# Kernel tuning notes

Measured on AMD Instinct MI355X. Metric: run time of the kernel, lower is better.

## Reference

```python
import jax, jax.numpy as jnp
import numpy as np

DN = ('NCHW', 'OIHW', 'NCHW')

def conv2d(x, w, b, stride, pad):
    y = jax.lax.conv_general_dilated(x, w, (stride, stride), [(pad, pad), (pad, pad)], dimension_numbers=DN)
    return y + b[None, :, None, None]

def convT2d(x, w, b, stride, pad):
    # w is torch ConvTranspose2d layout (in, out, kh, kw)
    k = w.shape[2]
    w2 = jnp.flip(w, (2, 3)).transpose(1, 0, 2, 3)  # -> (out, in, kh, kw)
    p = k - 1 - pad
    y = jax.lax.conv_general_dilated(x, w2, (1, 1), [(p, p), (p, p)], lhs_dilation=(stride, stride), dimension_numbers=DN)
    return y + b[None, :, None, None]

def setup_inputs() -> dict:
    key = jax.random.key(0)
    ks = jax.random.split(key, 24)
    s = 0.05
    inp = {
        'x': jax.random.uniform(ks[0], (16, 3, 256, 256), jnp.float32),
        'enc_w1': jax.random.normal(ks[1], (64, 3, 4, 4)) * s,   'enc_b1': jnp.zeros((64,)),
        'enc_w2': jax.random.normal(ks[2], (128, 64, 4, 4)) * s, 'enc_b2': jnp.zeros((128,)),
        'enc_w3': jax.random.normal(ks[3], (256, 128, 3, 3)) * s,'enc_b3': jnp.zeros((256,)),
        'enc_w4': jax.random.normal(ks[4], (256, 256, 3, 3)) * s,'enc_b4': jnp.zeros((256,)),
        'codebooks': jax.random.normal(ks[5], (4, 1024, 256)) * s,
        'dec_w1': jax.random.normal(ks[6], (128, 256, 3, 3)) * s,'dec_b1': jnp.zeros((128,)),
        'dec_w2': jax.random.normal(ks[7], (128, 64, 4, 4)) * s, 'dec_b2': jnp.zeros((64,)),
        'dec_w3': jax.random.normal(ks[8], (64, 64, 4, 4)) * s,  'dec_b3': jnp.zeros((64,)),
        'dec_w4': jax.random.normal(ks[9], (64, 3, 4, 4)) * s,   'dec_b4': jnp.zeros((3,)),
    }
    return inp

def residual_vq(zf, codebooks):
    # zf: (N, C) flattened tokens; codebooks: (Q, K, C)
    residual = zf
    q_out = jnp.zeros_like(zf)
    losses, inds = [], []
    for i in range(codebooks.shape[0]):
        cb = codebooks[i]  # (K, C)
        # squared distance up to a constant |r|^2 term (same argmin)
        d = jnp.sum(cb * cb, -1)[None, :] - 2.0 * (residual @ cb.T)  # (N, K)
        idx = jnp.argmin(d, axis=-1)  # (N,)
        q = cb[idx]  # (N, C)
        losses.append(jnp.mean((jax.lax.stop_gradient(q) - residual) ** 2))
        q_st = residual + jax.lax.stop_gradient(q - residual)  # straight-through
        q_out = q_out + q_st
        residual = residual - jax.lax.stop_gradient(q)
        inds.append(idx)
    return q_out, jnp.stack(inds, -1), jnp.stack(losses)

def reference(x, enc_w1, enc_b1, enc_w2, enc_b2, enc_w3, enc_b3, enc_w4, enc_b4,
              codebooks, dec_w1, dec_b1, dec_w2, dec_b2, dec_w3, dec_b3, dec_w4, dec_b4):
    h = jax.nn.relu(conv2d(x, enc_w1, enc_b1, 2, 1))
    h = jax.nn.relu(conv2d(h, enc_w2, enc_b2, 2, 1))
    h = jax.nn.relu(conv2d(h, enc_w3, enc_b3, 1, 1))
    z = conv2d(h, enc_w4, enc_b4, 1, 1)  # (B, C, H, W)
    B, C, H, W = z.shape
    zf = z.transpose(0, 2, 3, 1).reshape(B * H * W, C)
    qf, idx, commit_loss = residual_vq(zf, codebooks)
    quantized = qf.reshape(B, H, W, C).transpose(0, 3, 1, 2)
    # indices: (B, HW, Q) -> permute(0,2,1) -> view(B, Q, H, W)
    Q = codebooks.shape[0]
    indices = idx.reshape(B, H * W, Q).transpose(0, 2, 1).reshape(B, Q, H, W)
    d = jax.nn.relu(conv2d(quantized, dec_w1, dec_b1, 1, 1))
    d = jax.nn.relu(convT2d(d, dec_w2, dec_b2, 2, 1))
    d = jax.nn.relu(convT2d(d, dec_w3, dec_b3, 2, 1))
    recon = jnp.tanh(convT2d(d, dec_w4, dec_b4, 2, 1))
    return (recon, indices, commit_loss, quantized)
```

## Files before the change

### kernel.cpp

```cpp
#include <hip/hip_runtime.h>
#include <cmath>


typedef unsigned short u16;
typedef unsigned int   u32;
typedef __attribute__((ext_vector_type(8))) short s16x8;
typedef __attribute__((ext_vector_type(4))) short s16x4;
typedef __attribute__((ext_vector_type(4))) float f32x4;
typedef __attribute__((address_space(1))) const u32 gu32;
typedef __attribute__((address_space(3))) u32 lu32;

__device__ __forceinline__ u16 f2bf(float v) {
  u32 b = __builtin_bit_cast(u32, v);
  b += 0x7FFFu + ((b >> 16) & 1u);
  return (u16)(b >> 16);
}
__device__ __forceinline__ float bf2f(u16 h) {
  u32 b = ((u32)h) << 16;
  return __builtin_bit_cast(float, b);
}

template<int RW>
__device__ __forceinline__ void load_row(const float* __restrict__ p, float* r) {
  if constexpr (RW == 5) {
    float4 a = *(const float4*)p;
    r[0]=a.x; r[1]=a.y; r[2]=a.z; r[3]=a.w; r[4]=p[4];
  } else if constexpr (RW == 6) {
    float4 a = *(const float4*)p; float2 b = *(const float2*)(p+4);
    r[0]=a.x; r[1]=a.y; r[2]=a.z; r[3]=a.w; r[4]=b.x; r[5]=b.y;
  } else if constexpr (RW == 10) {
    float4 a = *(const float4*)p; float4 b = *(const float4*)(p+4);
    float2 c = *(const float2*)(p+8);
    r[0]=a.x; r[1]=a.y; r[2]=a.z; r[3]=a.w;
    r[4]=b.x; r[5]=b.y; r[6]=b.z; r[7]=b.w; r[8]=c.x; r[9]=c.y;
  }
}

template<int OCT, int SPTH, int SPTW, int KH, int KW, int S, int ACT>
__global__ __launch_bounds__(256) void conv_tiled(
    const float* __restrict__ in, const float* __restrict__ wgt,
    const float* __restrict__ bias, float* __restrict__ out,
    int N, int Cin, int Hin, int Win, int Cout, int WT,
    int padY, int padX,
    long outBase, long outNStride, long outCStride, long outYStride, long outXStride)
{
  constexpr int CK   = 8;
  constexpr int IH   = (SPTH-1)*S + KH;
  constexpr int IWr  = (SPTW-1)*S + KW;
  constexpr int IW   = (IWr + 3) & ~3;
  constexpr int TAPS = KH*KW;
  constexpr int WST  = (OCT==64) ? 68 : 5;
  constexpr int LOC  = (OCT==64) ? 16 : 4;
  constexpr int OPT  = OCT/LOC;
  constexpr int RW   = 3*S + KW;
  constexpr int EPW  = (OCT==64) ? 65 : 257;
  constexpr int SP   = SPTH*SPTW;
  constexpr int STG  = CK*IH*IW + CK*TAPS*WST;
  constexpr int SMEMN = (STG > OCT*EPW) ? STG : OCT*EPW;
  __shared__ float smem[SMEMN];
  float* s_in = smem;
  float* s_w  = smem + CK*IH*IW;

  const int tid  = threadIdx.x;
  const int tile = blockIdx.x, ocb = blockIdx.y, n = blockIdx.z;
  const int oy0 = (tile / WT) * SPTH, ox0 = (tile % WT) * SPTW;
  const int ol  = tid % LOC;
  const int g   = tid / LOC;
  const int s0  = g * 4;
  const int sy  = s0 / SPTW, sx0 = s0 % SPTW;
  const int iy0 = oy0*S - padY, ix0 = ox0*S - padX;

  float acc[OPT][4];
#pragma unroll
  for (int o = 0; o < OPT; ++o)
#pragma unroll
    for (int j = 0; j < 4; ++j) acc[o][j] = 0.f;

  for (int c0 = 0; c0 < Cin; c0 += CK) {
    __syncthreads();
    for (int i = tid; i < CK*IH*IW; i += 256) {
      int c = i / (IH*IW), r2 = i % (IH*IW);
      int iy = r2 / IW, ix = r2 % IW;
      int gy = iy0 + iy, gx = ix0 + ix;
      float v = 0.f;
      if (c0 + c < Cin && (unsigned)gy < (unsigned)Hin && (unsigned)gx < (unsigned)Win)
        v = in[(((long)n*Cin + c0 + c)*Hin + gy)*Win + gx];
      s_in[i] = v;
    }
    for (int i = tid; i < OCT*CK*TAPS; i += 256) {
      int o = i / (CK*TAPS), ct = i % (CK*TAPS);
      int oc = ocb*OCT + o, ci = c0 + ct / TAPS;
      float v = 0.f;
      if (oc < Cout && ci < Cin)
        v = wgt[((long)oc*Cin + ci)*TAPS + (ct % TAPS)];
      s_w[ct*WST + o] = v;
    }
    __syncthreads();

    for (int c = 0; c < CK; ++c) {
#pragma unroll
      for (int ky = 0; ky < KH; ++ky) {
        float r[RW];
        load_row<RW>(&s_in[c*(IH*IW) + (sy*S + ky)*IW + sx0*S], r);
#pragma unroll
        for (int kx = 0; kx < KW; ++kx) {
          if constexpr (OCT == 64) {
            float4 w4 = *(const float4*)&s_w[(c*TAPS + ky*KW + kx)*WST + ol*4];
            float wv[4] = {w4.x, w4.y, w4.z, w4.w};
#pragma unroll
            for (int o = 0; o < 4; ++o)
#pragma unroll
              for (int j = 0; j < 4; ++j)
                acc[o][j] = fmaf(wv[o], r[j*S + kx], acc[o][j]);
          } else {
            float w = s_w[(c*TAPS + ky*KW + kx)*WST + ol];
#pragma unroll
            for (int j = 0; j < 4; ++j)
              acc[0][j] = fmaf(w, r[j*S + kx], acc[0][j]);
          }
        }
      }
    }
  }

  __syncthreads();
#pragma unroll
  for (int o = 0; o < OPT; ++o) {
    int oc = ocb*OCT + ol*OPT + o;
    float b = (oc < Cout) ? bias[oc] : 0.f;
#pragma unroll
    for (int j = 0; j < 4; ++j) {
      float v = acc[o][j] + b;
      if constexpr (ACT == 1) v = fmaxf(v, 0.f);
      else if constexpr (ACT == 2) v = tanhf(v);
      smem[(ol*OPT + o)*EPW + s0 + j] = v;
    }
  }
  __syncthreads();
  for (int i = tid; i < OCT*SP; i += 256) {
    int o = i / SP, sp = i % SP;
    int oc = ocb*OCT + o;
    if (oc < Cout) {
      int syy = sp / SPTW, sxx = sp % SPTW;
      long off = outBase + (long)n*outNStride + (long)oc*outCStride
               + (long)(oy0 + syy)*outYStride + (long)(ox0 + sxx)*outXStride;
      out[off] = smem[o*EPW + sp];
    }
  }
}

template<int NP>
__global__ __launch_bounds__(256) void to_nhwc_bf16(const float* __restrict__ in,
    u16* __restrict__ t, long PS, int C, int HW) {
  __shared__ float sm[32][65];
  const int n = blockIdx.z, c0 = blockIdx.y << 5, w0 = blockIdx.x << 6;
  const long ibase = ((long)n * C + c0) * HW + w0;
  for (int i = threadIdx.x; i < 2048; i += 256) {
    int c = i >> 6, w = i & 63;
    sm[c][w] = in[ibase + (long)c * HW + w];
  }
  __syncthreads();
  for (int i = threadIdx.x; i < 512; i += 256) {
    int w = i >> 3, c4 = (i & 7) << 2;
    short hv[4], mv[4], lv[4];
#pragma unroll
    for (int q = 0; q < 4; ++q) {
      float v = sm[c4 + q][w];
      u16 h = f2bf(v); hv[q] = (short)h;
      float r1 = v - bf2f(h);
      u16 m = f2bf(r1); mv[q] = (short)m;
      if (NP == 3) lv[q] = (short)f2bf(r1 - bf2f(m));
    }
    int scr = c4 ^ ((w & 3) << 3);
    long o = ((long)n * HW + w0 + w) * C + c0 + scr;
    *(s16x4*)(t + o)      = *(s16x4*)hv;
    *(s16x4*)(t + PS + o) = *(s16x4*)mv;
    if (NP == 3) *(s16x4*)(t + 2*PS + o) = *(s16x4*)lv;
  }
}

template<int NP>
__global__ void wsplit(const float* __restrict__ w, u16* __restrict__ dst,
                       long PS, int Cout, int Cin, int TAPS) {
  int total = TAPS * Cout * Cin;
  for (int i = blockIdx.x * 256 + threadIdx.x; i < total; i += gridDim.x * 256) {
    int ic = i % Cin; int rest = i / Cin; int oc = rest % Cout; int tap = rest / Cout;
    float v = w[((long)oc * Cin + ic) * TAPS + tap];
    u16 h = f2bf(v);
    dst[i] = h;
    float r1 = v - bf2f(h);
    u16 m = f2bf(r1);
    dst[PS + i] = m;
    if (NP == 3) dst[2*PS + i] = f2bf(r1 - bf2f(m));
  }
}

__global__ void cbsplit(const float* __restrict__ cb, u16* __restrict__ dst) {
  int total = 4 * 1024 * 256;
  for (int i = blockIdx.x * 256 + threadIdx.x; i < total; i += gridDim.x * 256) {
    int l = i >> 18, kc = i & 262143;
    float v = cb[i];
    u16 h = f2bf(v);
    float r1 = v - bf2f(h);
    u16 m = f2bf(r1);
    long b = (long)l * 786432 + kc;
    dst[b] = h;
    dst[b + 262144] = m;
    dst[b + 524288] = f2bf(r1 - bf2f(m));
  }
}

template<int KH, int KW, int ACT, int NW>
__global__ __launch_bounds__(256, 3) void conv_mfma(
    const u16* __restrict__ act, long actPS,
    const u16* __restrict__ wgt, long wgtPS,
    const float* __restrict__ bias, float* __restrict__ out,
    int Cin, int H, int W, int Cout, int WT, int padY, int padX,
    long outBase, long outNS, long outCS, long outYS, long outXS)
{
  constexpr int PH = 8 + KH - 1, PW = 8 + KW - 1;
  constexpr int PPOS = PH * PW;
  constexpr int NU = (PPOS + 15) / 16;
  constexpr int PLANE = NU * 512;
  constexpr int BUFU = NW * PLANE;
  constexpr int TAPS = KH * KW;
  constexpr int PATCHB = 2 * BUFU * 2;
  constexpr int SFLOATS = ((PATCHB > 17408) ? PATCHB : 17408) / 4;
  __shared__ float smem[SFLOATS];
  u16* patch = (u16*)smem;
  float* s_ep = smem;

  const int tid = threadIdx.x;
  const int wv = tid >> 6, ln = tid & 63;
  const int r = ln & 15, kb = ln >> 4;
  const int tile = blockIdx.x, ocb = blockIdx.y, n = blockIdx.z;
  const int oy0 = (tile / WT) * 8, ox0 = (tile % WT) * 8;
  const int y0p = oy0 - padY, x0p = ox0 - padX;
  const bool border = (y0p < 0) | (x0p < 0) | (y0p + PH > H) | (x0p + PW > W);

  const int sp = ln >> 2;
  const int cs = (ln & 3) * 8;

  int aoff0[4], xb[4];
#pragma unroll
  for (int m = 0; m < 4; ++m) {
    int pos = m * 16 + r;
    int sy = pos >> 3, sx = pos & 7;
    aoff0[m] = (sy * PW + sx) * 32;
    xb[m] = x0p + sx;
  }

  f32x4 acc[4] = {};
  f32x4 acc2[4] = {};

  const long actNS = (long)H * W * Cin;
  const long tstep = (long)Cout * Cin;
  const u16* wrow = wgt + (long)(ocb * 64 + wv * 16 + r) * Cin + kb * 8;
  const u16* gact = act + (long)n * actNS;

  if (border) {
    for (int i = tid; i < 2 * BUFU / 8; i += 256)
      ((int4*)patch)[i] = make_int4(0, 0, 0, 0);
  }
  __syncthreads();

  auto stage = [&](int b, int c0) {
    u16* bb = patch + b * BUFU;
    for (int u = wv; u < NW * NU; u += 4) {
      int pl = u / NU, up = u - pl * NU;
      u16* dst = bb + pl * PLANE + up * 512;
      int p = up * 16 + sp;
      int py = p / PW, px = p - py * PW;
      int gy = y0p + py, gx = x0p + px;
      bool valid = (p < PPOS) & ((unsigned)gy < (unsigned)H) & ((unsigned)gx < (unsigned)W);
      if (valid) {
        const u16* src = gact + pl * actPS + ((long)gy * W + gx) * Cin + c0 + cs;
        __builtin_amdgcn_global_load_lds((const gu32*)src, (lu32*)dst, 16, 0, 0);
      }
    }
  };

  stage(0, 0);
  int buf = 0;
  for (int c0 = 0; c0 < Cin; c0 += 32) {
    __syncthreads();
    s16x8 Bb[2][NW];
    {
      const u16* base = wrow + c0;
#pragma unroll
      for (int p = 0; p < NW; ++p) Bb[0][p] = *(const s16x8*)(base + p * wgtPS);
    }
    if (c0 + 32 < Cin) stage(buf ^ 1, c0 + 32);
    const u16* pb = patch + buf * BUFU;
#pragma unroll
    for (int t = 0; t < TAPS; ++t) {
      if (t + 1 < TAPS) {
        const u16* base = wrow + (long)(t + 1) * tstep + c0;
#pragma unroll
        for (int p = 0; p < NW; ++p)
          Bb[(t + 1) & 1][p] = *(const s16x8*)(base + p * wgtPS);
      }
      const int ky = t / KW, kx = t % KW;
#pragma unroll
      for (int m = 0; m < 4; ++m) {
        const int key = (xb[m] + kx) & 3;
        const int aoff = aoff0[m] + (ky * PW + kx) * 32 + ((kb ^ key) * 8);
        s16x8 a[NW];
#pragma unroll
        for (int p = 0; p < NW; ++p)
          a[p] = *(const s16x8*)(pb + p * PLANE + aoff);
        acc[m] = __builtin_amdgcn_mfma_f32_16x16x32_bf16(a[0], Bb[t & 1][0], acc[m], 0, 0, 0);
        if constexpr (NW == 2) {
          acc[m] = __builtin_amdgcn_mfma_f32_16x16x32_bf16(a[1], Bb[t & 1][0], acc[m], 0, 0, 0);
          acc[m] = __builtin_amdgcn_mfma_f32_16x16x32_bf16(a[0], Bb[t & 1][1], acc[m], 0, 0, 0);
        } else {
          acc2[m] = __builtin_amdgcn_mfma_f32_16x16x32_bf16(a[1], Bb[t & 1][0], acc2[m], 0, 0, 0);
          acc2[m] = __builtin_amdgcn_mfma_f32_16x16x32_bf16(a[0], Bb[t & 1][1], acc2[m], 0, 0, 0);
          acc2[m] = __builtin_amdgcn_mfma_f32_16x16x32_bf16(a[2], Bb[t & 1][0], acc2[m], 0, 0, 0);
          acc2[m] = __builtin_amdgcn_mfma_f32_16x16x32_bf16(a[0], Bb[t & 1][2], acc2[m], 0, 0, 0);
          acc2[m] = __builtin_amdgcn_mfma_f32_16x16x32_bf16(a[1], Bb[t & 1][1], acc2[m], 0, 0, 0);
        }
      }
    }
    buf ^= 1;
  }

  __syncthreads();
  const float bsv = bias[ocb * 64 + wv * 16 + r];
#pragma unroll
  for (int m = 0; m < 4; ++m) {
    f32x4 v = acc[m];
#pragma unroll
    for (int j = 0; j < 4; ++j) {
      float x = v[j];
      if constexpr (NW == 3) x += acc2[m][j];
      x += bsv;
      if (ACT == 1) x = fmaxf(x, 0.f);
      v[j] = x;
    }
    *(f32x4*)&s_ep[(wv * 16 + r) * 68 + m * 16 + kb * 4] = v;
  }
  __syncthreads();
  for (int i = tid; i < 4096; i += 256) {
    int oc = i >> 6, p2 = i & 63;
    int syy = p2 >> 3, sxx = p2 & 7;
    long off = outBase + (long)n * outNS + (long)(ocb * 64 + oc) * outCS
             + (long)(oy0 + syy) * outYS + (long)(ox0 + sxx) * outXS;
    out[off] = s_ep[oc * 68 + p2];
  }
}

__global__ void rearrange_convT(const float* __restrict__ w, float* __restrict__ wp,
                                int Cin, int Cout) {
  int total = 4*Cout*Cin*4;
  for (int idx = blockIdx.x*256 + threadIdx.x; idx < total; idx += gridDim.x*256) {
    int e = idx & 1, d = (idx >> 1) & 1;
    int r = idx >> 2;
    int ic = r % Cin; r /= Cin;
    int oc = r % Cout; int p = r / Cout;
    int py = p >> 1, px = p & 1;
    int ky = py ? (d ? 0 : 2) : (d ? 1 : 3);
    int kx = px ? (e ? 0 : 2) : (e ? 1 : 3);
    wp[idx] = w[((ic*Cout + oc)*4 + ky)*4 + kx];
  }
}

__global__ __launch_bounds__(256) void cb_norm(const float* __restrict__ cb,
                                               float* __restrict__ outn) {
  int row = blockIdx.x;
  float v = cb[(long)row*256 + threadIdx.x];
  v *= v;
  for (int off = 32; off; off >>= 1) v += __shfl_down(v, off, 64);
  __shared__ float sr[4];
  if ((threadIdx.x & 63) == 0) sr[threadIdx.x >> 6] = v;
  __syncthreads();
  if (threadIdx.x == 0) outn[row] = sr[0] + sr[1] + sr[2] + sr[3];
}

__global__ void zero4(float* __restrict__ p) {
  if (threadIdx.x < 4) p[threadIdx.x] = 0.f;
}

__global__ __launch_bounds__(256) void transpose_zt(const float* __restrict__ z,
                                                    float* __restrict__ zt,
                                                    float* __restrict__ res,
                                                    u16* __restrict__ resp) {
  __shared__ float t[32][33];
  int b = blockIdx.z, c0 = blockIdx.y*32, hw0 = blockIdx.x*32;
  for (int i = threadIdx.x; i < 1024; i += 256) {
    int cc = i >> 5, ww = i & 31;
    t[cc][ww] = z[((long)(b*256 + c0 + cc) << 12) + hw0 + ww];
  }
  __syncthreads();
  for (int i = threadIdx.x; i < 1024; i += 256) {
    int ww = i >> 5, cc = i & 31;
    float v = t[cc][ww];
    long o = ((long)(b*4096 + hw0 + ww) << 8) + c0 + cc;
    zt[o] = v; res[o] = v;
    u16 h = f2bf(v);
    float r1 = v - bf2f(h);
    u16 m = f2bf(r1);
    resp[o] = h;
    resp[16777216L + o] = m;
    resp[33554432L + o] = f2bf(r1 - bf2f(m));
  }
}

__global__ __launch_bounds__(256) void make_quantized(const float* __restrict__ zt,
                                                      const float* __restrict__ res,
                                                      float* __restrict__ q) {
  __shared__ float t[32][33];
  int b = blockIdx.z, c0 = blockIdx.y*32, hw0 = blockIdx.x*32;
  for (int i = threadIdx.x; i < 1024; i += 256) {
    int tt = i >> 5, cc = i & 31;
    long o = ((long)(b*4096 + hw0 + tt) << 8) + c0 + cc;
    t[cc][tt] = zt[o] - res[o];
  }
  __syncthreads();
  for (int i = threadIdx.x; i < 1024; i += 256) {
    int cc = i >> 5, ww = i & 31;
    q[((long)(b*256 + c0 + cc) << 12) + hw0 + ww] = t[cc][ww];
  }
}

template<bool WP>
__global__ __launch_bounds__(256, 2) void vq_mfma(
    const u16* __restrict__ cbp, const float* __restrict__ cb,
    const float* __restrict__ cbn,
    float* __restrict__ res, u16* __restrict__ resp,
    float* __restrict__ idx_out, float* __restrict__ loss_out)
{
  __shared__ u16  sB[2][6144];
  __shared__ int   s_idx[64];
  __shared__ float s_ls[4];
  const int tid = threadIdx.x;
  const int wv = tid >> 6, ln = tid & 63;
  const int r = ln & 15, kb = ln >> 4;
  const long t0 = (long)blockIdx.x * 64;
  const long tok = t0 + wv * 16 + r;

  s16x8 A[3][8];
#pragma unroll
  for (int p = 0; p < 3; ++p)
#pragma unroll
    for (int ks = 0; ks < 8; ++ks)
      A[p][ks] = *(const s16x8*)(resp + (long)p * 16777216 + tok * 256 + ks * 32 + kb * 8);

  const int srr = ln >> 2;
  const int sks = ((ln & 3) ^ (srr & 3)) * 8;
  auto stageB = [&](int b, int n0, int ks) {
    const int c0 = ks * 32;
#pragma unroll
    for (int i = 0; i < 3; ++i) {
      int u = wv + 4 * i;
      int p = u >> 2, g = u & 3;
      const u16* src = cbp + (long)p * 262144
                     + (long)(n0 + g * 16 + srr) * 256 + c0 + sks;
      u16* dst = (u16*)&sB[b][p * 2048 + g * 512];
      __builtin_amdgcn_global_load_lds((const gu32*)src, (lu32*)dst, 16, 0, 0);
    }
  };

  float bv[4]; int bi[4];
#pragma unroll
  for (int j = 0; j < 4; ++j) { bv[j] = 3.4e38f; bi[j] = 0; }

  const int swk = (kb ^ (r & 3)) * 8;
  stageB(0, 0, 0);
  int buf = 0;
  for (int n0 = 0; n0 < 1024; n0 += 64) {
    f32x4 acc[4] = {};
    f32x4 acc2[4] = {};
#pragma unroll
    for (int ks = 0; ks < 8; ++ks) {
      __syncthreads();
      if (ks < 7)             stageB(buf ^ 1, n0, ks + 1);
      else if (n0 + 64 < 1024) stageB(buf ^ 1, n0 + 64, 0);
#pragma unroll
      for (int nt = 0; nt < 4; ++nt) {
        const u16* bb = &sB[buf][(nt * 16 + r) * 32 + swk];
        s16x8 b0 = *(const s16x8*)(bb);
        s16x8 b1 = *(const s16x8*)(bb + 2048);
        s16x8 b2 = *(const s16x8*)(bb + 4096);
        acc[nt]  = __builtin_amdgcn_mfma_f32_16x16x32_bf16(A[0][ks], b0, acc[nt], 0, 0, 0);
        acc2[nt] = __builtin_amdgcn_mfma_f32_16x16x32_bf16(A[1][ks], b0, acc2[nt], 0, 0, 0);
        acc2[nt] = __builtin_amdgcn_mfma_f32_16x16x32_bf16(A[0][ks], b1, acc2[nt], 0, 0, 0);
        acc2[nt] = __builtin_amdgcn_mfma_f32_16x16x32_bf16(A[2][ks], b0, acc2[nt], 0, 0, 0);
        acc2[nt] = __builtin_amdgcn_mfma_f32_16x16x32_bf16(A[0][ks], b2, acc2[nt], 0, 0, 0);
        acc2[nt] = __builtin_amdgcn_mfma_f32_16x16x32_bf16(A[1][ks], b1, acc2[nt], 0, 0, 0);
      }
      buf ^= 1;
    }
#pragma unroll
    for (int nt = 0; nt < 4; ++nt) {
      int code = n0 + nt * 16 + r;
      float cn = cbn[code];
#pragma unroll
      for (int j = 0; j < 4; ++j) {
        float d = cn - 2.f * (acc[nt][j] + acc2[nt][j]);
        if (d < bv[j]) { bv[j] = d; bi[j] = code; }
      }
    }
  }

#pragma unroll
  for (int m = 1; m < 16; m <<= 1) {
#pragma unroll
    for (int j = 0; j < 4; ++j) {
      float ov = __shfl_xor(bv[j], m, 64);
      int   oi = __shfl_xor(bi[j], m, 64);
      if (ov < bv[j] || (ov == bv[j] && oi < bi[j])) { bv[j] = ov; bi[j] = oi; }
    }
  }
  if (r == 0) {
#pragma unroll
    for (int j = 0; j < 4; ++j) s_idx[wv * 16 + kb * 4 + j] = bi[j];
  }
  __syncthreads();

  const int c = tid;
  float lsum = 0.f;
  for (int m2 = 0; m2 < 64; ++m2) {
    int w = s_idx[m2];
    long ro = (t0 + m2) * 256 + c;
    float nv = res[ro] - cb[(long)w * 256 + c];
    res[ro] = nv;
    lsum += nv * nv;
    if (WP) {
      u16 h = f2bf(nv);
      float r1 = nv - bf2f(h);
      u16 mm = f2bf(r1);
      resp[ro] = h;
      resp[16777216L + ro] = mm;
      resp[33554432L + ro] = f2bf(r1 - bf2f(mm));
    }
  }
  for (int off = 32; off; off >>= 1) lsum += __shfl_down(lsum, off, 64);
  if (ln == 0) s_ls[wv] = lsum;
  __syncthreads();
  if (tid == 0)
    atomicAdd(loss_out, (s_ls[0] + s_ls[1] + s_ls[2] + s_ls[3]) * (1.f/(65536.f*256.f)));
  if (tid < 64) {
    long tglob = t0 + tid;
    int b = (int)(tglob >> 12), hw = (int)(tglob & 4095);
    idx_out[(long)b * 16384 + hw] = (float)s_idx[tid];
  }
}

extern "C" void kernel_launch(void* const* d_in, const int* in_sizes, int n_in,
                              void* d_out, int out_size, void* d_ws, size_t ws_size,
                              hipStream_t stream) {
  const float* x      = (const float*)d_in[0];
  const float* ew1    = (const float*)d_in[1];
  const float* eb1    = (const float*)d_in[2];
  const float* ew2    = (const float*)d_in[3];
  const float* eb2    = (const float*)d_in[4];
  const float* ew3    = (const float*)d_in[5];
  const float* eb3    = (const float*)d_in[6];
  const float* ew4    = (const float*)d_in[7];
  const float* eb4    = (const float*)d_in[8];
  const float* cbooks = (const float*)d_in[9];
  const float* dw1    = (const float*)d_in[10];
  const float* db1    = (const float*)d_in[11];
  const float* dw2    = (const float*)d_in[12];
  const float* db2    = (const float*)d_in[13];
  const float* dw3    = (const float*)d_in[14];
  const float* db3    = (const float*)d_in[15];
  const float* dw4    = (const float*)d_in[16];
  const float* db4    = (const float*)d_in[17];

  float* out = (float*)d_out;
  float* o_recon = out;
  float* o_idx   = out + 12582912;
  float* o_loss  = out + 12845056;
  float* o_q     = out + 12845060;

  float* ws  = (float*)d_ws;
  float* wp2 = ws;
  float* wp3 = ws + 131072;
  float* wp4 = ws + 196608;
  float* cbn = ws + 199680;
  u16* wu   = (u16*)(ws + 203776);
  u16* e3w  = wu;
  u16* e4w  = wu + 884736;
  u16* d1w  = wu + 2654208;
  u16* t2w  = wu + 3244032;
  u16* t3w  = wu + 3506176;

  const long DA = 2097152;
  float* h1  = ws + DA;
  float* h2  = ws + DA + 16777216;
  float* h3  = ws + DA;
  float* z   = ws + DA + 58720256;
  float* zt  = ws + DA;
  float* res = ws + DA + 16777216;
  u16* resp  = (u16*)(ws + DA + 33554432);
  u16* cbp   = (u16*)(ws + DA + 75497472);
  float* d1  = ws + DA;
  float* d2  = ws + DA + 16777216;
  float* d3  = ws + DA + 16777216;
  u16* A3 = (u16*)(ws + DA + 25165824);
  u16* A4 = (u16*)(ws + DA + 16777216);
  u16* D1 = (u16*)(ws + DA + 33554432);
  u16* D2 = (u16*)(ws + DA + 8388608);
  u16* D3 = (u16*)(ws + DA);

  rearrange_convT<<<256, 256, 0, stream>>>(dw2, wp2, 128, 64);
  rearrange_convT<<<256, 256, 0, stream>>>(dw3, wp3, 64, 64);
  rearrange_convT<<<16, 256, 0, stream>>>(dw4, wp4, 64, 3);
  cb_norm<<<4096, 256, 0, stream>>>(cbooks, cbn);
  cbsplit<<<512, 256, 0, stream>>>(cbooks, cbp);
  zero4<<<1, 64, 0, stream>>>(o_loss);
  wsplit<3><<<256, 256, 0, stream>>>(ew3, e3w, 294912L, 256, 128, 9);
  wsplit<3><<<256, 256, 0, stream>>>(ew4, e4w, 589824L, 256, 256, 9);
  wsplit<2><<<256, 256, 0, stream>>>(dw1, d1w, 294912L, 128, 256, 9);
  for (int p = 0; p < 4; ++p) {
    wsplit<2><<<64, 256, 0, stream>>>(wp2 + p*32768, t2w + p*65536, 32768L, 64, 128, 4);
    wsplit<2><<<64, 256, 0, stream>>>(wp3 + p*16384, t3w + p*32768, 16384L, 64, 64, 4);
  }

  conv_tiled<64,8,8,4,4,2,1><<<dim3(256,1,16), 256, 0, stream>>>(
      x, ew1, eb1, h1, 16, 3, 256, 256, 64, 16, 1, 1,
      0L, 1048576L, 16384L, 128L, 1L);
  conv_tiled<64,8,8,4,4,2,1><<<dim3(64,2,16), 256, 0, stream>>>(
      h1, ew2, eb2, h2, 16, 64, 128, 128, 128, 8, 1, 1,
      0L, 524288L, 4096L, 64L, 1L);

  to_nhwc_bf16<3><<<dim3(64,4,16), 256, 0, stream>>>(h2, A3, 8388608L, 128, 4096);
  conv_mfma<3,3,1,3><<<dim3(64,4,16), 256, 0, stream>>>(
      A3, 8388608L, e3w, 294912L, eb3, h3,
      128, 64, 64, 256, 8, 1, 1, 0L, 1048576L, 4096L, 64L, 1L);

  to_nhwc_bf16<3><<<dim3(64,8,16), 256, 0, stream>>>(h3, A4, 16777216L, 256, 4096);
  conv_mfma<3,3,0,3><<<dim3(64,4,16), 256, 0, stream>>>(
      A4, 16777216L, e4w, 589824L, eb4, z,
      256, 64, 64, 256, 8, 1, 1, 0L, 1048576L, 4096L, 64L, 1L);

  transpose_zt<<<dim3(128,8,16), 256, 0, stream>>>(z, zt, res, resp);
  for (int l = 0; l < 3; ++l)
    vq_mfma<true><<<1024, 256, 0, stream>>>(cbp + (long)l*786432,
        cbooks + (long)l*262144, cbn + l*1024, res, resp,
        o_idx + l*4096, o_loss + l);
  vq_mfma<false><<<1024, 256, 0, stream>>>(cbp + 3L*786432,
      cbooks + 3L*262144, cbn + 3*1024, res, resp,
      o_idx + 3*4096, o_loss + 3);
  make_quantized<<<dim3(128,8,16), 256, 0, stream>>>(zt, res, o_q);

  to_nhwc_bf16<2><<<dim3(64,8,16), 256, 0, stream>>>(o_q, D1, 16777216L, 256, 4096);
  conv_mfma<3,3,1,2><<<dim3(64,2,16), 256, 0, stream>>>(
      D1, 16777216L, d1w, 294912L, db1, d1,
      256, 64, 64, 128, 8, 1, 1, 0L, 524288L, 4096L, 64L, 1L);

  to_nhwc_bf16<2><<<dim3(64,4,16), 256, 0, stream>>>(d1, D2, 8388608L, 128, 4096);
  for (int p = 0; p < 4; ++p) {
    int py = p >> 1, px = p & 1;
    conv_mfma<2,2,1,2><<<dim3(64,1,16), 256, 0, stream>>>(
        D2, 8388608L, t2w + p*65536, 32768L, db2, d2,
        128, 64, 64, 64, 8, 1-py, 1-px,
        (long)(py*128 + px), 1048576L, 16384L, 256L, 2L);
  }

  to_nhwc_bf16<2><<<dim3(256,2,16), 256, 0, stream>>>(d2, D3, 16777216L, 64, 16384);
  for (int p = 0; p < 4; ++p) {
    int py = p >> 1, px = p & 1;
    conv_mfma<2,2,1,2><<<dim3(256,1,16), 256, 0, stream>>>(
        D3, 16777216L, t3w + p*32768, 16384L, db3, d3,
        64, 128, 128, 64, 16, 1-py, 1-px,
        (long)(py*256 + px), 4194304L, 65536L, 512L, 2L);
  }

  for (int p = 0; p < 4; ++p) {
    int py = p >> 1, px = p & 1;
    conv_tiled<4,16,16,2,2,1,2><<<dim3(256,1,16), 256, 0, stream>>>(
        d3, wp4 + p*768, db4, o_recon, 16, 64, 256, 256, 3, 16, 1-py, 1-px,
        (long)(py*512 + px), 786432L, 262144L, 1024L, 2L);
  }
  (void)in_sizes; (void)n_in; (void)out_size; (void)ws_size;
}
```

Measured before the change: 4.142 ms.

## Run stride-2 encoder convs as space-to-depth 2x2 MFMA convolutions

The first two stride-2 4x4 encoder convolutions move off the scalar conv_tiled kernel. The input is rearranged by space-to-depth parity into padded NHWC three-way bf16 split buffers, and the weights are regrouped the same way. This turns each conv into a stride-1 2x2 convolution that the existing MFMA conv kernel can run, so the FMA-bound scalar work goes to matrix cores. The cost is two extra rearrange kernels, more workspace traffic, and padding layer 1 from 3 input channels up to 32.

```diff
diff --git a/kernel.cpp b/kernel.cpp
--- a/kernel.cpp
+++ b/kernel.cpp
@@ -179,6 +179,53 @@
   }
 }
 
+template<int C, int CBLK>
+__global__ __launch_bounds__(256) void par_nhwc(
+    const float* __restrict__ in, u16* __restrict__ t, long PS,
+    int Hin, int Win, int HP)
+{
+  constexpr int CP = 4 * CBLK;
+  constexpr int QPV = CP / 4;
+  __shared__ float sm[2][C][66];
+  const int n = blockIdx.z, u = blockIdx.y, v0 = blockIdx.x * 32;
+  const long ib = (long)n * C * Hin * Win;
+  for (int i = threadIdx.x; i < 2 * C * 66; i += 256) {
+    int j = i % 66; int c = (i / 66) % C; int rr = i / (66 * C);
+    int gy = rr ? 2 * u : 2 * u - 1;
+    int gx = 2 * v0 - 1 + j;
+    float val = 0.f;
+    if ((unsigned)gy < (unsigned)Hin && (unsigned)gx < (unsigned)Win)
+      val = in[ib + ((long)c * Hin + gy) * Win + gx];
+    sm[rr][c][j] = val;
+  }
+  __syncthreads();
+  for (int q = threadIdx.x; q < 32 * QPV; q += 256) {
+    int v = v0 + q / QPV;
+    if (v >= HP) continue;
+    int cq = (q % QPV) * 4;
+    int g = cq / CBLK, cb = cq % CBLK;
+    int ry = g >> 1, rx = g & 1;
+    int j = 2 * (v - v0) + rx;
+    short hv[4], mv[4], lv[4];
+#pragma unroll
+    for (int p = 0; p < 4; ++p) {
+      int c = cb + p;
+      float val = (c < C) ? sm[ry][c][j] : 0.f;
+      u16 h = f2bf(val); hv[p] = (short)h;
+      float r1 = val - bf2f(h);
+      u16 m = f2bf(r1); mv[p] = (short)m;
+      lv[p] = (short)f2bf(r1 - bf2f(m));
+    }
+    int cc = g * CBLK + cb;
+    int grp = cc >> 5;
+    int slot = (cc & 31) ^ ((v & 3) << 3);
+    long o = (((long)n * HP + u) * HP + v) * CP + (grp << 5) + slot;
+    *(s16x4*)(t + o)        = *(s16x4*)hv;
+    *(s16x4*)(t + PS + o)   = *(s16x4*)mv;
+    *(s16x4*)(t + 2*PS + o) = *(s16x4*)lv;
+  }
+}
+
 template<int NP>
 __global__ void wsplit(const float* __restrict__ w, u16* __restrict__ dst,
                        long PS, int Cout, int Cin, int TAPS) {
@@ -192,6 +239,25 @@
     u16 m = f2bf(r1);
     dst[PS + i] = m;
     if (NP == 3) dst[2*PS + i] = f2bf(r1 - bf2f(m));
+  }
+}
+
+template<int C, int CBLK>
+__global__ void wsplit_s2(const float* __restrict__ w, u16* __restrict__ dst,
+                          long PS, int Cout) {
+  constexpr int CP = 4 * CBLK;
+  int total = 4 * Cout * CP;
+  for (int i = blockIdx.x * 256 + threadIdx.x; i < total; i += gridDim.x * 256) {
+    int cc = i % CP; int oc = (i / CP) % Cout; int t = i / (CP * Cout);
+    int d = t >> 1, e = t & 1;
+    int g = cc / CBLK, c = cc % CBLK;
+    int ry = g >> 1, rx = g & 1;
+    int ky = 2 * d + ry, kx = 2 * e + rx;
+    float v = (c < C) ? w[((long)(oc * C + c) * 4 + ky) * 4 + kx] : 0.f;
+    u16 h = f2bf(v); dst[i] = h;
+    float r1 = v - bf2f(h);
+    u16 m = f2bf(r1); dst[PS + i] = m;
+    dst[2*PS + i] = f2bf(r1 - bf2f(m));
   }
 }
 
@@ -588,8 +654,12 @@
   u16* t3w  = wu + 3506176;
 
   const long DA = 2097152;
-  float* h1  = ws + DA;
-  float* h2  = ws + DA + 16777216;
+  u16*  P1  = (u16*)(ws + DA);
+  float* h1 = ws + DA + 12780288;
+  u16*  P2  = (u16*)(ws + DA + 29557504);
+  float* h2 = ws + DA + 55515904;
+  u16* w1p  = (u16*)(ws + DA + 72000000);
+  u16* w2p  = w1p + 24576;
   float* h3  = ws + DA;
   float* z   = ws + DA + 58720256;
   float* zt  = ws + DA;
@@ -611,6 +681,8 @@
   cb_norm<<<4096, 256, 0, stream>>>(cbooks, cbn);
   cbsplit<<<512, 256, 0, stream>>>(cbooks, cbp);
   zero4<<<1, 64, 0, stream>>>(o_loss);
+  wsplit_s2<3,8><<<32, 256, 0, stream>>>(ew1, w1p, 8192L, 64);
+  wsplit_s2<64,64><<<128, 256, 0, stream>>>(ew2, w2p, 131072L, 128);
   wsplit<3><<<256, 256, 0, stream>>>(ew3, e3w, 294912L, 256, 128, 9);
   wsplit<3><<<256, 256, 0, stream>>>(ew4, e4w, 589824L, 256, 256, 9);
   wsplit<2><<<256, 256, 0, stream>>>(dw1, d1w, 294912L, 128, 256, 9);
@@ -619,12 +691,15 @@
     wsplit<2><<<64, 256, 0, stream>>>(wp3 + p*16384, t3w + p*32768, 16384L, 64, 64, 4);
   }
 
-  conv_tiled<64,8,8,4,4,2,1><<<dim3(256,1,16), 256, 0, stream>>>(
-      x, ew1, eb1, h1, 16, 3, 256, 256, 64, 16, 1, 1,
-      0L, 1048576L, 16384L, 128L, 1L);
-  conv_tiled<64,8,8,4,4,2,1><<<dim3(64,2,16), 256, 0, stream>>>(
-      h1, ew2, eb2, h2, 16, 64, 128, 128, 128, 8, 1, 1,
-      0L, 524288L, 4096L, 64L, 1L);
+  par_nhwc<3,8><<<dim3(5,129,16), 256, 0, stream>>>(x, P1, 8520192L, 256, 256, 129);
+  conv_mfma<2,2,1,3><<<dim3(256,1,16), 256, 0, stream>>>(
+      P1, 8520192L, w1p, 8192L, eb1, h1,
+      32, 129, 129, 64, 16, 0, 0, 0L, 1048576L, 16384L, 128L, 1L);
+
+  par_nhwc<64,64><<<dim3(3,65,16), 256, 0, stream>>>(h1, P2, 17305600L, 128, 128, 65);
+  conv_mfma<2,2,1,3><<<dim3(64,2,16), 256, 0, stream>>>(
+      P2, 17305600L, w2p, 131072L, eb2, h2,
+      256, 65, 65, 128, 8, 0, 0, 0L, 524288L, 4096L, 64L, 1L);
 
   to_nhwc_bf16<3><<<dim3(64,4,16), 256, 0, stream>>>(h2, A3, 8388608L, 128, 4096);
   conv_mfma<3,3,1,3><<<dim3(64,4,16), 256, 0, stream>>>(
```

New measurement: 3.651 ms. 1.13x faster.
